# Optimization experiments

Hardware: AMD Instinct MI355X
Metric: run time of the kernel (lower is better)

## Reference

```python
import jax, jax.numpy as jnp
import numpy as np

N, E, D, H, L, G, OUT = 16384, 65536, 64, 128, 3, 512, 128
EPS = 1e-5


def setup_inputs() -> dict:
    key = jax.random.key(0)
    ks = jax.random.split(key, 12)
    s = 0.05  # small init to keep res+ stack stable
    return {
        "x": jax.random.normal(ks[0], (N, D), jnp.float32),
        "edge_index": jax.random.randint(ks[1], (2, E), 0, N, jnp.int32),
        "edge_attr": jax.random.normal(ks[2], (E, D), jnp.float32),
        "batch": jnp.sort(jax.random.randint(ks[3], (N,), 0, G, jnp.int32)),
        # per-layer params, stacked on leading layer dim L
        "ln_scale": jnp.ones((L, D), jnp.float32),
        "ln_bias": jnp.zeros((L, D), jnp.float32),
        "W1": jax.random.normal(ks[4], (L, D, H), jnp.float32) * s,
        "b1": jnp.zeros((L, H), jnp.float32),
        "W2": jax.random.normal(ks[5], (L, H, D * D), jnp.float32) * s,
        "b2": jnp.zeros((L, D * D), jnp.float32),
        "root": jax.random.normal(ks[6], (L, D, D), jnp.float32) * s,
        "conv_b": jnp.zeros((L, D), jnp.float32),
        # head params
        "dense_W": jax.random.normal(ks[7], (D, D), jnp.float32) * s,
        "dense_b": jnp.zeros((D,), jnp.float32),
        "out_W": jax.random.normal(ks[8], (D, OUT), jnp.float32) * s,
        "out_b": jnp.zeros((OUT,), jnp.float32),
    }


def _layer_norm(h, scale, bias):
    mu = jnp.mean(h, axis=-1, keepdims=True)
    var = jnp.mean((h - mu) ** 2, axis=-1, keepdims=True)
    return (h - mu) * jax.lax.rsqrt(var + EPS) * scale + bias


def _gnn_layer(x, edge_index, edge_attr, ln_scale, ln_bias, W1, b1, W2, b2, root, conv_b):
    # DeepGCNLayer block='res+': h = conv(dropout(act(norm(x)))); return x + h
    # (dropout is identity in eval/reference)
    h = jax.nn.leaky_relu(_layer_norm(x, ln_scale, ln_bias))
    src, dst = edge_index[0], edge_index[1]
    # NNConv: per-edge DxD weight from edge MLP (MapE2NxN with LeakyReLU)
    w = jax.nn.leaky_relu(edge_attr @ W1 + b1) @ W2 + b2       # [E, D*D]
    w = w.reshape(-1, D, D)                                     # [E, D, D]
    msg = jnp.einsum('ed,edf->ef', h[src], w)                   # [E, D]
    num = jax.ops.segment_sum(msg, dst, num_segments=N)         # [N, D]
    deg = jax.ops.segment_sum(jnp.ones((msg.shape[0],), msg.dtype), dst, num_segments=N)
    agg = num / jnp.maximum(deg, 1.0)[:, None]                  # mean aggregation
    conv = agg + h @ root + conv_b                              # root weight + bias
    return x + conv


def reference(x, edge_index, edge_attr, batch, ln_scale, ln_bias, W1, b1, W2, b2,
              root, conv_b, dense_W, dense_b, out_W, out_b):
    for l in range(L):
        x = _gnn_layer(x, edge_index, edge_attr, ln_scale[l], ln_bias[l],
                       W1[l], b1[l], W2[l], b2[l], root[l], conv_b[l])
    x = x @ dense_W + dense_b
    # global_mean_pool over graphs
    num = jax.ops.segment_sum(x, batch, num_segments=G)
    cnt = jax.ops.segment_sum(jnp.ones((x.shape[0],), x.dtype), batch, num_segments=G)
    pooled = num / jnp.maximum(cnt, 1.0)[:, None]
    pooled = jax.nn.leaky_relu(pooled)
    return pooled @ out_W + out_b
```

## Files before the change

kernel.cpp:

```cpp
#include <hip/hip_runtime.h>
#include <hip/hip_bf16.h>

#define NN 16384
#define EE 65536
#define DD 64
#define HH 128
#define LL 3
#define GG 512
#define OUTD 128
#define NEG 0.01f

#define CHUNK 8192
#define KSEG 8


typedef __attribute__((ext_vector_type(8))) short short8;
typedef __attribute__((ext_vector_type(4))) float f32x4;

__device__ __forceinline__ float leaky(float x){ return x > 0.f ? x : NEG * x; }
__device__ __forceinline__ unsigned short f2bf(float f){
  union { float f; unsigned int u; } v; v.f = f;
  unsigned int r = v.u + 0x7fffu + ((v.u >> 16) & 1u);
  return (unsigned short)(r >> 16);
}

__global__ void k_init(const float* x_in, float* x_cur, int* deg, int* cursor,
                       int* cnt, float* pooled){
  int i = blockIdx.x*256 + threadIdx.x;
  x_cur[i] = x_in[i];
  if (i < NN){ deg[i] = 0; cursor[i] = 0; }
  if (i < GG) cnt[i] = 0;
  if (i < GG*DD) pooled[i] = 0.f;
}

__global__ void k_degcnt(const int* ei, const int* batch, int* deg, int* cnt){
  int e = blockIdx.x*256 + threadIdx.x;
  atomicAdd(&deg[ei[EE + e]], 1);
  if (e < NN) atomicAdd(&cnt[batch[e]], 1);
}
__global__ void k_scan(const int* deg, int* row_ptr){
  __shared__ int part[256];
  int t = threadIdx.x;
  int base = t*64; int s = 0;
  for (int i=0;i<64;++i) s += deg[base+i];
  part[t] = s; __syncthreads();
  for (int off=1; off<256; off<<=1){
    int v = (t>=off)?part[t-off]:0; __syncthreads();
    part[t] += v; __syncthreads();
  }
  int run = (t==0)?0:part[t-1];
  if (t==0) row_ptr[0] = 0;
  for (int i=0;i<64;++i){ run += deg[base+i]; row_ptr[base+i+1] = run; }
}
__global__ void k_fill(const int* ei, const int* row_ptr, int* cursor,
                       int* edge_id, int* src_sorted){
  int e = blockIdx.x*256 + threadIdx.x;
  if (e < EE){
    int d = ei[EE + e];
    int pos = row_ptr[d] + atomicAdd(&cursor[d], 1);
    edge_id[pos] = e;
    src_sorted[pos] = ei[e];
  }
}

#define CV_A (EE*DD)
#define CV_B (LL*HH*DD)
#define CV_C (LL*64*8192)
__global__ void k_convert(const float* ea, const float* W1, const float* W2,
                          unsigned short* eab, unsigned short* W1T, unsigned short* W2T){
  int idx = blockIdx.x*256 + threadIdx.x;
  if (idx < CV_A){
    eab[idx] = f2bf(ea[idx]);
  } else if (idx < CV_A + CV_B){
    int i = idx - CV_A;
    int l = i >> 13, r = i & 8191;
    int j = r >> 6, d = r & 63;
    W1T[i] = f2bf(W1[(size_t)l*DD*HH + d*HH + j]);
  } else {
    int i = idx - CV_A - CV_B;
    int l = i >> 19, rem = i & ((1<<19)-1);
    int f = rem >> 13, c = rem & 8191;
    int kd = 128*((c>>3)&63) + 64*(c>>12) + 8*((c>>9)&7) + (c&7);
    W2T[i] = f2bf(W2[(size_t)l*HH*DD*DD + (size_t)kd*DD + f]);
  }
}

__global__ __launch_bounds__(256, 2)
void k_lnmlp(const float* x, const float* scale, const float* bias, float* h,
             const unsigned short* eab, const unsigned short* W1T, const float* b1,
             unsigned short* ug, int l){
  __shared__ __align__(16) unsigned short a_lds[128][72];
  __shared__ __align__(16) unsigned short b_lds[128][72];
  __shared__ __align__(16) unsigned short c_lds[128][136];
  int t = threadIdx.x;
  if (blockIdx.x < NN/4){
    int lane = t & 63, nl = t >> 6;
    int n = blockIdx.x*4 + nl;
    float v = x[(size_t)n*DD + lane];
    float s = v;
    for (int m=1;m<64;m<<=1) s += __shfl_xor(s, m, 64);
    float mu = s * (1.0f/64.0f);
    float dv = v - mu;
    float q = dv*dv;
    for (int m=1;m<64;m<<=1) q += __shfl_xor(q, m, 64);
    float var = q * (1.0f/64.0f);
    float w = dv * rsqrtf(var + 1e-5f) * scale[l*DD + lane] + bias[l*DD + lane];
    h[(size_t)n*DD + lane] = leaky(w);
    return;
  }
  int e0 = (blockIdx.x - NN/4) * 128;
  {
    int row = t >> 1, col = (t & 1) * 32;
    const float4* sa = (const float4*)(eab + (size_t)(e0 + row)*DD + col);
    const float4* sb = (const float4*)(W1T + (size_t)l*HH*DD + (size_t)row*DD + col);
    #pragma unroll
    for (int i=0;i<4;++i){
      *(float4*)&a_lds[row][col + 8*i] = sa[i];
      *(float4*)&b_lds[row][col + 8*i] = sb[i];
    }
  }
  __syncthreads();
  int wave = t >> 6, lane = t & 63;
  int m0 = (wave >> 1) * 64, j0 = (wave & 1) * 64;
  int lr = lane & 15, lq = lane >> 4;
  f32x4 acc[4][4];
  #pragma unroll
  for (int a=0;a<4;++a)
    #pragma unroll
    for (int b=0;b<4;++b) acc[a][b] = (f32x4){0.f,0.f,0.f,0.f};
  #pragma unroll
  for (int ks=0; ks<2; ++ks){
    short8 av[4];
    #pragma unroll
    for (int mt=0; mt<4; ++mt) av[mt] = *(const short8*)&a_lds[m0 + mt*16 + lr][ks*32 + lq*8];
    #pragma unroll
    for (int jt=0; jt<4; ++jt){
      short8 bv = *(const short8*)&b_lds[j0 + jt*16 + lr][ks*32 + lq*8];
      #pragma unroll
      for (int mt=0; mt<4; ++mt)
        acc[mt][jt] = __builtin_amdgcn_mfma_f32_16x16x32_bf16(av[mt], bv, acc[mt][jt], 0, 0, 0);
    }
  }
  #pragma unroll
  for (int mt=0; mt<4; ++mt)
    #pragma unroll
    for (int jt=0; jt<4; ++jt){
      int col = j0 + jt*16 + lr;
      float bj = b1[l*HH + col];
      #pragma unroll
      for (int r=0; r<4; ++r){
        int row = m0 + mt*16 + lq*4 + r;
        c_lds[row][col] = f2bf(leaky(acc[mt][jt][r] + bj));
      }
    }
  __syncthreads();
  {
    int row = t >> 1, half = t & 1;
    float4* dst = (float4*)(ug + (size_t)(e0 + row)*HH + half*64);
    #pragma unroll
    for (int i=0;i<8;++i) dst[i] = *(const float4*)&c_lds[row][half*64 + 8*i];
  }
}

__global__ __launch_bounds__(256, 2)
void k_sbuild2(const unsigned short* ug, const float* h, const int* row_ptr,
               const int* edge_id, const int* src_sorted,
               unsigned short* S, float* Hs, int chunk_base){
  int t = threadIdx.x, wave = t >> 6, lane = t & 63;
  int nloc = blockIdx.x*4 + wave;
  int n = chunk_base + nloc;
  int r0 = row_ptr[n], r1 = row_ptr[n+1];
  float acc0[64], acc1[64];
  #pragma unroll
  for (int d=0; d<64; ++d){ acc0[d] = 0.f; acc1[d] = 0.f; }
  float hs = 0.f;
  int pos = r0;
  for (; pos + 4 <= r1; pos += 4){
    int e0 = edge_id[pos],   e1 = edge_id[pos+1],   e2 = edge_id[pos+2],   e3 = edge_id[pos+3];
    int s0 = src_sorted[pos],s1 = src_sorted[pos+1],s2 = src_sorted[pos+2],s3 = src_sorted[pos+3];
    float hv0 = h[(size_t)s0*DD + lane];
    float hv1 = h[(size_t)s1*DD + lane];
    float hv2 = h[(size_t)s2*DD + lane];
    float hv3 = h[(size_t)s3*DD + lane];
    unsigned int q0 = *(const unsigned int*)(ug + (size_t)e0*HH + 2*lane);
    unsigned int q1 = *(const unsigned int*)(ug + (size_t)e1*HH + 2*lane);
    unsigned int q2 = *(const unsigned int*)(ug + (size_t)e2*HH + 2*lane);
    unsigned int q3 = *(const unsigned int*)(ug + (size_t)e3*HH + 2*lane);
    float u00 = __uint_as_float(q0 << 16), u01 = __uint_as_float(q0 & 0xFFFF0000u);
    float u10 = __uint_as_float(q1 << 16), u11 = __uint_as_float(q1 & 0xFFFF0000u);
    float u20 = __uint_as_float(q2 << 16), u21 = __uint_as_float(q2 & 0xFFFF0000u);
    float u30 = __uint_as_float(q3 << 16), u31 = __uint_as_float(q3 & 0xFFFF0000u);
    hs += hv0 + hv1 + hv2 + hv3;
    int h0 = __float_as_int(hv0), h1 = __float_as_int(hv1);
    int h2 = __float_as_int(hv2), h3 = __float_as_int(hv3);
    #pragma unroll
    for (int d=0; d<64; ++d){
      float sh0 = __int_as_float(__builtin_amdgcn_readlane(h0, d));
      float sh1 = __int_as_float(__builtin_amdgcn_readlane(h1, d));
      float sh2 = __int_as_float(__builtin_amdgcn_readlane(h2, d));
      float sh3 = __int_as_float(__builtin_amdgcn_readlane(h3, d));
      acc0[d] += u00*sh0; acc1[d] += u01*sh0;
      acc0[d] += u10*sh1; acc1[d] += u11*sh1;
      acc0[d] += u20*sh2; acc1[d] += u21*sh2;
      acc0[d] += u30*sh3; acc1[d] += u31*sh3;
    }
  }
  for (; pos < r1; ++pos){
    int e = edge_id[pos];
    int s = src_sorted[pos];
    float hv = h[(size_t)s*DD + lane];
    unsigned int up = *(const unsigned int*)(ug + (size_t)e*HH + 2*lane);
    float u0 = __uint_as_float(up << 16);
    float u1 = __uint_as_float(up & 0xFFFF0000u);
    hs += hv;
    int hvi = __float_as_int(hv);
    #pragma unroll
    for (int d=0; d<64; ++d){
      float sh = __int_as_float(__builtin_amdgcn_readlane(hvi, d));
      acc0[d] += u0 * sh;
      acc1[d] += u1 * sh;
    }
  }
  float4* Srow = (float4*)(S + (size_t)nloc*8192);
  #pragma unroll
  for (int k2=0; k2<2; ++k2){
    union { unsigned int u[32]; float4 v[8]; } buf;
    #pragma unroll
    for (int i=0;i<32;++i){
      float a0 = k2 ? acc1[2*i]   : acc0[2*i];
      float a1 = k2 ? acc1[2*i+1] : acc0[2*i+1];
      buf.u[i] = (unsigned int)f2bf(a0) | ((unsigned int)f2bf(a1) << 16);
    }
    #pragma unroll
    for (int i=0;i<8;++i)
      Srow[(k2*8 + i)*64 + lane] = buf.v[i];
  }
  Hs[(size_t)n*DD + lane] = hs;
}

__global__ __launch_bounds__(256, 4)
void k_gemm(const unsigned short* S, const unsigned short* W2T,
            float* num_part, int chunk_base){
  __shared__ __align__(16) unsigned short a_lds[64][136];
  __shared__ __align__(16) unsigned short b_lds[64][136];
  int t = threadIdx.x;
  int wave = t >> 6, lane = t & 63;
  int rowblk = blockIdx.x, kseg = blockIdx.y;
  int lr = lane & 15, lq = lane >> 4;
  f32x4 acc[4];
  #pragma unroll
  for (int b=0;b<4;++b) acc[b] = (f32x4){0.f,0.f,0.f,0.f};
  int m0 = wave * 16;
  int r = t >> 2, q = t & 3;
  for (int it = 0; it < 8; ++it){
    int kbase = kseg*1024 + it*128;
    {
      const float4* sa = (const float4*)(S + (size_t)(rowblk*64 + r)*8192 + kbase);
      const float4* sb = (const float4*)(W2T + (size_t)r*8192 + kbase);
      float4* da = (float4*)&a_lds[r][0];
      float4* db = (float4*)&b_lds[r][0];
      #pragma unroll
      for (int i=0;i<4;++i){ da[q + 4*i] = sa[q + 4*i]; db[q + 4*i] = sb[q + 4*i]; }
    }
    __syncthreads();
    #pragma unroll
    for (int kk=0; kk<128; kk+=32){
      short8 av = *(const short8*)&a_lds[m0 + lr][kk + lq*8];
      #pragma unroll
      for (int ft=0; ft<4; ++ft){
        short8 bv = *(const short8*)&b_lds[ft*16 + lr][kk + lq*8];
        acc[ft] = __builtin_amdgcn_mfma_f32_16x16x32_bf16(av, bv, acc[ft], 0, 0, 0);
      }
    }
    __syncthreads();
  }
  float* dstp = num_part + (size_t)kseg*NN*DD;
  #pragma unroll
  for (int ft=0; ft<4; ++ft)
    #pragma unroll
    for (int rr=0; rr<4; ++rr){
      int m = m0 + lq*4 + rr;
      int f = ft*16 + lr;
      int n = chunk_base + rowblk*64 + m;
      dstp[(size_t)n*DD + f] = acc[ft][rr];
    }
}

__global__ void k_update(float* x, const float* num_part, const float* h, const float* Hs,
                         const int* deg, const float* root, const float* b2,
                         const float* conv_b, int l){
  __shared__ float rl[64][64];
  __shared__ float b2l[64][64];
  __shared__ float hrow[4][64];
  __shared__ float hsrow[4][64];
  int t = threadIdx.x;
  int f = t & 63, nl = t >> 6;
  for (int idx=t; idx<4096; idx+=256){
    rl[idx>>6][idx&63]  = root[(size_t)l*4096 + idx];
    b2l[idx>>6][idx&63] = b2[(size_t)l*4096 + idx];
  }
  int n = blockIdx.x*4 + nl;
  hrow[nl][f]  = h[(size_t)n*DD + f];
  hsrow[nl][f] = Hs[(size_t)n*DD + f];
  __syncthreads();
  float dg = (float)deg[n]; if (dg < 1.f) dg = 1.f;
  float nsum = 0.f;
  #pragma unroll
  for (int p=0; p<KSEG; ++p) nsum += num_part[(size_t)p*NN*DD + (size_t)n*DD + f];
  float acc = x[(size_t)n*DD + f] + nsum/dg + conv_b[l*DD + f];
  #pragma unroll
  for (int d=0; d<64; ++d)
    acc += hrow[nl][d]*rl[d][f] + hsrow[nl][d]*b2l[d][f];
  x[(size_t)n*DD + f] = acc;
}

__global__ void k_dense_pool(const float* x, const float* dW, const float* db,
                             const int* batch, float* pooled){
  __shared__ float wl[64][64];
  __shared__ float xrow[4][64];
  int t = threadIdx.x;
  int f = t & 63, nl = t >> 6;
  for (int idx=t; idx<4096; idx+=256) wl[idx>>6][idx&63] = dW[idx];
  int n = blockIdx.x*4 + nl;
  xrow[nl][f] = x[(size_t)n*DD + f];
  __syncthreads();
  float acc = db[f];
  #pragma unroll
  for (int d=0; d<64; ++d) acc += xrow[nl][d]*wl[d][f];
  atomicAdd(&pooled[(size_t)batch[n]*DD + f], acc);
}

__global__ void k_final(const float* pooled, const int* cnt, const float* oW,
                        const float* ob, float* out){
  __shared__ float p[64];
  int g = blockIdx.x, t = threadIdx.x;
  if (t < 64){
    float c = (float)cnt[g]; if (c < 1.f) c = 1.f;
    p[t] = leaky(pooled[(size_t)g*DD + t] / c);
  }
  __syncthreads();
  float acc = ob[t];
  #pragma unroll
  for (int f=0; f<64; ++f) acc += p[f]*oW[(size_t)f*OUTD + t];
  out[(size_t)g*OUTD + t] = acc;
}

__global__ void k_diag(float* out, float val, int n){
  int i = blockIdx.x*256 + threadIdx.x;
  if (i < n) out[i] = (i==0) ? val : 0.f;
}

extern "C" void kernel_launch(void* const* d_in, const int* in_sizes, int n_in,
                              void* d_out, int out_size, void* d_ws, size_t ws_size,
                              hipStream_t stream){
  const float* x_in  = (const float*)d_in[0];
  const int*   ei    = (const int*)d_in[1];
  const float* ea    = (const float*)d_in[2];
  const int*   batch = (const int*)d_in[3];
  const float* ln_s  = (const float*)d_in[4];
  const float* ln_b  = (const float*)d_in[5];
  const float* W1    = (const float*)d_in[6];
  const float* b1    = (const float*)d_in[7];
  const float* W2    = (const float*)d_in[8];
  const float* b2    = (const float*)d_in[9];
  const float* root  = (const float*)d_in[10];
  const float* convb = (const float*)d_in[11];
  const float* dW    = (const float*)d_in[12];
  const float* db    = (const float*)d_in[13];
  const float* oW    = (const float*)d_in[14];
  const float* ob    = (const float*)d_in[15];
  float* out = (float*)d_out;

  char* ws = (char*)d_ws;
  size_t off = 0;
  auto alloc = [&](size_t bytes)->char*{
    char* p = ws + off; off = (off + bytes + 255) & ~(size_t)255; return p;
  };
  float* x_cur  = (float*)alloc((size_t)NN*DD*4);
  float* h      = (float*)alloc((size_t)NN*DD*4);
  unsigned short* ug  = (unsigned short*)alloc((size_t)EE*HH*2);
  float* num_part = (float*)alloc((size_t)KSEG*NN*DD*4);
  float* Hs     = (float*)alloc((size_t)NN*DD*4);
  unsigned short* S   = (unsigned short*)alloc((size_t)CHUNK*8192*2);
  unsigned short* W2T = (unsigned short*)alloc((size_t)LL*8192*64*2);
  unsigned short* eab = (unsigned short*)alloc((size_t)EE*DD*2);
  unsigned short* W1T = (unsigned short*)alloc((size_t)LL*HH*DD*2);
  int* deg     = (int*)alloc((size_t)NN*4);
  int* row_ptr = (int*)alloc((size_t)(NN+1)*4);
  int* cursor  = (int*)alloc((size_t)NN*4);
  int* edge_id = (int*)alloc((size_t)EE*4);
  int* src_sorted = (int*)alloc((size_t)EE*4);
  int* cnt     = (int*)alloc((size_t)GG*4);
  float* pooled= (float*)alloc((size_t)GG*DD*4);
  size_t needed = off;
  if (ws_size < needed){
    k_diag<<<(out_size+255)/256, 256, 0, stream>>>(out, (float)ws_size, out_size);
    return;
  }

  k_init   <<<NN*DD/256, 256, 0, stream>>>(x_in, x_cur, deg, cursor, cnt, pooled);
  k_degcnt <<<EE/256, 256, 0, stream>>>(ei, batch, deg, cnt);
  k_scan   <<<1, 256, 0, stream>>>(deg, row_ptr);
  k_fill   <<<EE/256, 256, 0, stream>>>(ei, row_ptr, cursor, edge_id, src_sorted);
  k_convert<<<(CV_A+CV_B+CV_C)/256, 256, 0, stream>>>(ea, W1, W2, eab, W1T, W2T);

  for (int l=0; l<LL; ++l){
    k_lnmlp<<<NN/4 + EE/128, 256, 0, stream>>>(x_cur, ln_s, ln_b, h, eab, W1T, b1, ug, l);
    for (int c=0; c<NN/CHUNK; ++c){
      k_sbuild2<<<CHUNK/4, 256, 0, stream>>>(ug, h, row_ptr, edge_id, src_sorted, S, Hs, c*CHUNK);
      k_gemm   <<<dim3(CHUNK/64, KSEG), 256, 0, stream>>>(S, W2T + (size_t)l*8192*64, num_part, c*CHUNK);
    }
    k_update<<<NN/4, 256, 0, stream>>>(x_cur, num_part, h, Hs, deg, root, b2, convb, l);
  }
  k_dense_pool<<<NN/4, 256, 0, stream>>>(x_cur, dW, db, batch, pooled);
  k_final     <<<GG, 128, 0, stream>>>(pooled, cnt, oW, ob, out);
}
```

Baseline: 609.4 us.

## Hoist edge MLP for all layers, fuse layernorm into update, split sbuild, enlarge gemm tile

The edge MLP does not depend on the layer input, so it now runs once for all three layers in a single launch before the layer loop, storing per-layer results in a tripled ug buffer. LayerNorm is fused into the init kernel and into the per-layer update kernel, which computes the next layer's h. The S-building kernel splits the two output halves across two waves per node, halving the accumulator registers and allowing higher occupancy at the cost of gathering h and ug twice. The GEMM tile grows to 128 rows per block with two MFMA row tiles per wave, which raises reuse of the W2T tile.

Result: slower. 644.7 us (+5.8%).

```diff
diff --git a/kernel.cpp b/kernel.cpp
--- a/kernel.cpp
+++ b/kernel.cpp
@@ -24,13 +24,27 @@
   return (unsigned short)(r >> 16);
 }
 
-__global__ void k_init(const float* x_in, float* x_cur, int* deg, int* cursor,
-                       int* cnt, float* pooled){
-  int i = blockIdx.x*256 + threadIdx.x;
-  x_cur[i] = x_in[i];
+__global__ void k_init_ln(const float* x_in, const float* scale, const float* bias,
+                          float* x_cur, float* h, int* deg, int* cursor,
+                          int* cnt, float* pooled){
+  int t = threadIdx.x;
+  int i = blockIdx.x*256 + t;
   if (i < NN){ deg[i] = 0; cursor[i] = 0; }
   if (i < GG) cnt[i] = 0;
   if (i < GG*DD) pooled[i] = 0.f;
+  int lane = t & 63, nl = t >> 6;
+  int n = blockIdx.x*4 + nl;
+  float v = x_in[(size_t)n*DD + lane];
+  x_cur[(size_t)n*DD + lane] = v;
+  float s = v;
+  for (int m=1;m<64;m<<=1) s += __shfl_xor(s, m, 64);
+  float mu = s * (1.0f/64.0f);
+  float dv = v - mu;
+  float q = dv*dv;
+  for (int m=1;m<64;m<<=1) q += __shfl_xor(q, m, 64);
+  float var = q * (1.0f/64.0f);
+  float w = dv * rsqrtf(var + 1e-5f) * scale[lane] + bias[lane];
+  h[(size_t)n*DD + lane] = leaky(w);
 }
 
 __global__ void k_degcnt(const int* ei, const int* batch, int* deg, int* cnt){
@@ -86,29 +100,14 @@
 }
 
 __global__ __launch_bounds__(256, 2)
-void k_lnmlp(const float* x, const float* scale, const float* bias, float* h,
-             const unsigned short* eab, const unsigned short* W1T, const float* b1,
-             unsigned short* ug, int l){
+void k_mlp3(const unsigned short* eab, const unsigned short* W1T, const float* b1,
+            unsigned short* ug){
   __shared__ __align__(16) unsigned short a_lds[128][72];
   __shared__ __align__(16) unsigned short b_lds[128][72];
   __shared__ __align__(16) unsigned short c_lds[128][136];
   int t = threadIdx.x;
-  if (blockIdx.x < NN/4){
-    int lane = t & 63, nl = t >> 6;
-    int n = blockIdx.x*4 + nl;
-    float v = x[(size_t)n*DD + lane];
-    float s = v;
-    for (int m=1;m<64;m<<=1) s += __shfl_xor(s, m, 64);
-    float mu = s * (1.0f/64.0f);
-    float dv = v - mu;
-    float q = dv*dv;
-    for (int m=1;m<64;m<<=1) q += __shfl_xor(q, m, 64);
-    float var = q * (1.0f/64.0f);
-    float w = dv * rsqrtf(var + 1e-5f) * scale[l*DD + lane] + bias[l*DD + lane];
-    h[(size_t)n*DD + lane] = leaky(w);
-    return;
-  }
-  int e0 = (blockIdx.x - NN/4) * 128;
+  int l  = blockIdx.x >> 9;
+  int e0 = (blockIdx.x & 511) * 128;
   {
     int row = t >> 1, col = (t & 1) * 32;
     const float4* sa = (const float4*)(eab + (size_t)(e0 + row)*DD + col);
@@ -156,23 +155,24 @@
   __syncthreads();
   {
     int row = t >> 1, half = t & 1;
-    float4* dst = (float4*)(ug + (size_t)(e0 + row)*HH + half*64);
+    float4* dst = (float4*)(ug + (size_t)l*EE*HH + (size_t)(e0 + row)*HH + half*64);
     #pragma unroll
     for (int i=0;i<8;++i) dst[i] = *(const float4*)&c_lds[row][half*64 + 8*i];
   }
 }
 
-__global__ __launch_bounds__(256, 2)
-void k_sbuild2(const unsigned short* ug, const float* h, const int* row_ptr,
+__global__ __launch_bounds__(256, 3)
+void k_sbuild3(const unsigned short* ug, const float* h, const int* row_ptr,
                const int* edge_id, const int* src_sorted,
                unsigned short* S, float* Hs, int chunk_base){
   int t = threadIdx.x, wave = t >> 6, lane = t & 63;
-  int nloc = blockIdx.x*4 + wave;
+  int q = wave & 1;
+  int nloc = blockIdx.x*2 + (wave >> 1);
   int n = chunk_base + nloc;
   int r0 = row_ptr[n], r1 = row_ptr[n+1];
-  float acc0[64], acc1[64];
-  #pragma unroll
-  for (int d=0; d<64; ++d){ acc0[d] = 0.f; acc1[d] = 0.f; }
+  float acc[64];
+  #pragma unroll
+  for (int d=0; d<64; ++d) acc[d] = 0.f;
   float hs = 0.f;
   int pos = r0;
   for (; pos + 4 <= r1; pos += 4){
@@ -186,10 +186,10 @@
     unsigned int q1 = *(const unsigned int*)(ug + (size_t)e1*HH + 2*lane);
     unsigned int q2 = *(const unsigned int*)(ug + (size_t)e2*HH + 2*lane);
     unsigned int q3 = *(const unsigned int*)(ug + (size_t)e3*HH + 2*lane);
-    float u00 = __uint_as_float(q0 << 16), u01 = __uint_as_float(q0 & 0xFFFF0000u);
-    float u10 = __uint_as_float(q1 << 16), u11 = __uint_as_float(q1 & 0xFFFF0000u);
-    float u20 = __uint_as_float(q2 << 16), u21 = __uint_as_float(q2 & 0xFFFF0000u);
-    float u30 = __uint_as_float(q3 << 16), u31 = __uint_as_float(q3 & 0xFFFF0000u);
+    float u0 = q ? __uint_as_float(q0 & 0xFFFF0000u) : __uint_as_float(q0 << 16);
+    float u1 = q ? __uint_as_float(q1 & 0xFFFF0000u) : __uint_as_float(q1 << 16);
+    float u2 = q ? __uint_as_float(q2 & 0xFFFF0000u) : __uint_as_float(q2 << 16);
+    float u3 = q ? __uint_as_float(q3 & 0xFFFF0000u) : __uint_as_float(q3 << 16);
     hs += hv0 + hv1 + hv2 + hv3;
     int h0 = __float_as_int(hv0), h1 = __float_as_int(hv1);
     int h2 = __float_as_int(hv2), h3 = __float_as_int(hv3);
@@ -199,10 +199,10 @@
       float sh1 = __int_as_float(__builtin_amdgcn_readlane(h1, d));
       float sh2 = __int_as_float(__builtin_amdgcn_readlane(h2, d));
       float sh3 = __int_as_float(__builtin_amdgcn_readlane(h3, d));
-      acc0[d] += u00*sh0; acc1[d] += u01*sh0;
-      acc0[d] += u10*sh1; acc1[d] += u11*sh1;
-      acc0[d] += u20*sh2; acc1[d] += u21*sh2;
-      acc0[d] += u30*sh3; acc1[d] += u31*sh3;
+      acc[d] += u0*sh0;
+      acc[d] += u1*sh1;
+      acc[d] += u2*sh2;
+      acc[d] += u3*sh3;
     }
   }
   for (; pos < r1; ++pos){
@@ -210,85 +210,87 @@
     int s = src_sorted[pos];
     float hv = h[(size_t)s*DD + lane];
     unsigned int up = *(const unsigned int*)(ug + (size_t)e*HH + 2*lane);
-    float u0 = __uint_as_float(up << 16);
-    float u1 = __uint_as_float(up & 0xFFFF0000u);
+    float u0 = q ? __uint_as_float(up & 0xFFFF0000u) : __uint_as_float(up << 16);
     hs += hv;
     int hvi = __float_as_int(hv);
     #pragma unroll
     for (int d=0; d<64; ++d){
       float sh = __int_as_float(__builtin_amdgcn_readlane(hvi, d));
-      acc0[d] += u0 * sh;
-      acc1[d] += u1 * sh;
+      acc[d] += u0 * sh;
     }
   }
   float4* Srow = (float4*)(S + (size_t)nloc*8192);
-  #pragma unroll
-  for (int k2=0; k2<2; ++k2){
-    union { unsigned int u[32]; float4 v[8]; } buf;
-    #pragma unroll
-    for (int i=0;i<32;++i){
-      float a0 = k2 ? acc1[2*i]   : acc0[2*i];
-      float a1 = k2 ? acc1[2*i+1] : acc0[2*i+1];
-      buf.u[i] = (unsigned int)f2bf(a0) | ((unsigned int)f2bf(a1) << 16);
-    }
-    #pragma unroll
-    for (int i=0;i<8;++i)
-      Srow[(k2*8 + i)*64 + lane] = buf.v[i];
-  }
-  Hs[(size_t)n*DD + lane] = hs;
-}
-
-__global__ __launch_bounds__(256, 4)
+  union { unsigned int u[32]; float4 v[8]; } buf;
+  #pragma unroll
+  for (int i=0;i<32;++i)
+    buf.u[i] = (unsigned int)f2bf(acc[2*i]) | ((unsigned int)f2bf(acc[2*i+1]) << 16);
+  #pragma unroll
+  for (int i=0;i<8;++i)
+    Srow[(q*8 + i)*64 + lane] = buf.v[i];
+  if (q == 0) Hs[(size_t)n*DD + lane] = hs;
+}
+
+__global__ __launch_bounds__(256, 2)
 void k_gemm(const unsigned short* S, const unsigned short* W2T,
             float* num_part, int chunk_base){
-  __shared__ __align__(16) unsigned short a_lds[64][136];
+  __shared__ __align__(16) unsigned short a_lds[128][136];
   __shared__ __align__(16) unsigned short b_lds[64][136];
   int t = threadIdx.x;
   int wave = t >> 6, lane = t & 63;
   int rowblk = blockIdx.x, kseg = blockIdx.y;
   int lr = lane & 15, lq = lane >> 4;
-  f32x4 acc[4];
-  #pragma unroll
-  for (int b=0;b<4;++b) acc[b] = (f32x4){0.f,0.f,0.f,0.f};
-  int m0 = wave * 16;
-  int r = t >> 2, q = t & 3;
+  f32x4 acc[2][4];
+  #pragma unroll
+  for (int a=0;a<2;++a)
+    #pragma unroll
+    for (int b=0;b<4;++b) acc[a][b] = (f32x4){0.f,0.f,0.f,0.f};
+  int m0 = wave * 32;
+  int ra = t >> 1, qa = t & 1;
+  int rb = t >> 2, qb = t & 3;
   for (int it = 0; it < 8; ++it){
     int kbase = kseg*1024 + it*128;
     {
-      const float4* sa = (const float4*)(S + (size_t)(rowblk*64 + r)*8192 + kbase);
-      const float4* sb = (const float4*)(W2T + (size_t)r*8192 + kbase);
-      float4* da = (float4*)&a_lds[r][0];
-      float4* db = (float4*)&b_lds[r][0];
-      #pragma unroll
-      for (int i=0;i<4;++i){ da[q + 4*i] = sa[q + 4*i]; db[q + 4*i] = sb[q + 4*i]; }
+      const float4* sa = (const float4*)(S + (size_t)(rowblk*128 + ra)*8192 + kbase + qa*64);
+      float4* da = (float4*)&a_lds[ra][qa*64];
+      #pragma unroll
+      for (int i=0;i<8;++i) da[i] = sa[i];
+      const float4* sb = (const float4*)(W2T + (size_t)rb*8192 + kbase + qb*32);
+      float4* db = (float4*)&b_lds[rb][qb*32];
+      #pragma unroll
+      for (int i=0;i<4;++i) db[i] = sb[i];
     }
     __syncthreads();
     #pragma unroll
     for (int kk=0; kk<128; kk+=32){
-      short8 av = *(const short8*)&a_lds[m0 + lr][kk + lq*8];
+      short8 a0 = *(const short8*)&a_lds[m0 + lr][kk + lq*8];
+      short8 a1 = *(const short8*)&a_lds[m0 + 16 + lr][kk + lq*8];
       #pragma unroll
       for (int ft=0; ft<4; ++ft){
         short8 bv = *(const short8*)&b_lds[ft*16 + lr][kk + lq*8];
-        acc[ft] = __builtin_amdgcn_mfma_f32_16x16x32_bf16(av, bv, acc[ft], 0, 0, 0);
+        acc[0][ft] = __builtin_amdgcn_mfma_f32_16x16x32_bf16(a0, bv, acc[0][ft], 0, 0, 0);
+        acc[1][ft] = __builtin_amdgcn_mfma_f32_16x16x32_bf16(a1, bv, acc[1][ft], 0, 0, 0);
       }
     }
     __syncthreads();
   }
   float* dstp = num_part + (size_t)kseg*NN*DD;
   #pragma unroll
-  for (int ft=0; ft<4; ++ft)
-    #pragma unroll
-    for (int rr=0; rr<4; ++rr){
-      int m = m0 + lq*4 + rr;
-      int f = ft*16 + lr;
-      int n = chunk_base + rowblk*64 + m;
-      dstp[(size_t)n*DD + f] = acc[ft][rr];
-    }
-}
-
-__global__ void k_update(float* x, const float* num_part, const float* h, const float* Hs,
-                         const int* deg, const float* root, const float* b2,
-                         const float* conv_b, int l){
+  for (int rt=0; rt<2; ++rt)
+    #pragma unroll
+    for (int ft=0; ft<4; ++ft)
+      #pragma unroll
+      for (int rr=0; rr<4; ++rr){
+        int m = m0 + rt*16 + lq*4 + rr;
+        int f = ft*16 + lr;
+        int n = chunk_base + rowblk*128 + m;
+        dstp[(size_t)n*DD + f] = acc[rt][ft][rr];
+      }
+}
+
+__global__ void k_update_ln(float* x, const float* num_part, float* h, const float* Hs,
+                            const int* deg, const float* root, const float* b2,
+                            const float* conv_b, const float* ln_s, const float* ln_b,
+                            int l, int do_ln){
   __shared__ float rl[64][64];
   __shared__ float b2l[64][64];
   __shared__ float hrow[4][64];
@@ -312,6 +314,18 @@
   for (int d=0; d<64; ++d)
     acc += hrow[nl][d]*rl[d][f] + hsrow[nl][d]*b2l[d][f];
   x[(size_t)n*DD + f] = acc;
+  if (do_ln){
+    int lp = l + 1;
+    float s = acc;
+    for (int m=1;m<64;m<<=1) s += __shfl_xor(s, m, 64);
+    float mu = s * (1.0f/64.0f);
+    float dv = acc - mu;
+    float qv = dv*dv;
+    for (int m=1;m<64;m<<=1) qv += __shfl_xor(qv, m, 64);
+    float var = qv * (1.0f/64.0f);
+    float w = dv * rsqrtf(var + 1e-5f) * ln_s[lp*DD + f] + ln_b[lp*DD + f];
+    h[(size_t)n*DD + f] = leaky(w);
+  }
 }
 
 __global__ void k_dense_pool(const float* x, const float* dW, const float* db,
@@ -378,7 +392,7 @@
   };
   float* x_cur  = (float*)alloc((size_t)NN*DD*4);
   float* h      = (float*)alloc((size_t)NN*DD*4);
-  unsigned short* ug  = (unsigned short*)alloc((size_t)EE*HH*2);
+  unsigned short* ug  = (unsigned short*)alloc((size_t)LL*EE*HH*2);
   float* num_part = (float*)alloc((size_t)KSEG*NN*DD*4);
   float* Hs     = (float*)alloc((size_t)NN*DD*4);
   unsigned short* S   = (unsigned short*)alloc((size_t)CHUNK*8192*2);
@@ -398,19 +412,21 @@
     return;
   }
 
-  k_init   <<<NN*DD/256, 256, 0, stream>>>(x_in, x_cur, deg, cursor, cnt, pooled);
+  k_init_ln<<<NN/4, 256, 0, stream>>>(x_in, ln_s, ln_b, x_cur, h, deg, cursor, cnt, pooled);
   k_degcnt <<<EE/256, 256, 0, stream>>>(ei, batch, deg, cnt);
   k_scan   <<<1, 256, 0, stream>>>(deg, row_ptr);
   k_fill   <<<EE/256, 256, 0, stream>>>(ei, row_ptr, cursor, edge_id, src_sorted);
   k_convert<<<(CV_A+CV_B+CV_C)/256, 256, 0, stream>>>(ea, W1, W2, eab, W1T, W2T);
+  k_mlp3   <<<LL*(EE/128), 256, 0, stream>>>(eab, W1T, b1, ug);
 
   for (int l=0; l<LL; ++l){
-    k_lnmlp<<<NN/4 + EE/128, 256, 0, stream>>>(x_cur, ln_s, ln_b, h, eab, W1T, b1, ug, l);
+    const unsigned short* ugl = ug + (size_t)l*EE*HH;
     for (int c=0; c<NN/CHUNK; ++c){
-      k_sbuild2<<<CHUNK/4, 256, 0, stream>>>(ug, h, row_ptr, edge_id, src_sorted, S, Hs, c*CHUNK);
-      k_gemm   <<<dim3(CHUNK/64, KSEG), 256, 0, stream>>>(S, W2T + (size_t)l*8192*64, num_part, c*CHUNK);
-    }
-    k_update<<<NN/4, 256, 0, stream>>>(x_cur, num_part, h, Hs, deg, root, b2, convb, l);
+      k_sbuild3<<<CHUNK/2, 256, 0, stream>>>(ugl, h, row_ptr, edge_id, src_sorted, S, Hs, c*CHUNK);
+      k_gemm   <<<dim3(CHUNK/128, KSEG), 256, 0, stream>>>(S, W2T + (size_t)l*8192*64, num_part, c*CHUNK);
+    }
+    k_update_ln<<<NN/4, 256, 0, stream>>>(x_cur, num_part, h, Hs, deg, root, b2, convb,
+                                          ln_s, ln_b, l, (l < LL-1) ? 1 : 0);
   }
   k_dense_pool<<<NN/4, 256, 0, stream>>>(x_cur, dW, db, batch, pooled);
   k_final     <<<GG, 128, 0, stream>>>(pooled, cnt, oW, ob, out);
```
